# Performance work log

Measured on AMD Instinct MI355X. Metric: run time of the kernel, lower is better.

The kernel has to match this reference:

```python
import jax, jax.numpy as jnp
import numpy as np

EPS = 1e-6

def _layernorm2d(x, w, b):
    # normalize over channel dim (axis=1) per (b,h,w)
    u = jnp.mean(x, axis=1, keepdims=True)
    s = jnp.mean((x - u) ** 2, axis=1, keepdims=True)
    xn = (x - u) / jnp.sqrt(s + EPS)
    return xn * w[None, :, None, None] + b[None, :, None, None]

def _conv1x1(x, w, b):
    # w: (O, C, 1, 1)
    y = jnp.einsum('bchw,oc->bohw', x, w[:, :, 0, 0])
    return y + b[None, :, None, None]

def _dwconv3x3(x, w):
    # w: (C, 1, 3, 3), groups = C, padding 1, no bias
    C = x.shape[1]
    return jax.lax.conv_general_dilated(
        x, w, window_strides=(1, 1), padding=((1, 1), (1, 1)),
        dimension_numbers=('NCHW', 'OIHW', 'NCHW'), feature_group_count=C)

def _linrec_scan(a, u, axis):
    # s_t = a_t * s_{t-1} + u_t via associative scan
    def comb(l, r):
        al, ul = l
        ar, ur = r
        return al * ar, ar * ul + ur
    return jax.lax.associative_scan(comb, (a, u), axis=axis)[1]

def _bidir_scan(z, a, b, g, axis):
    u = b * z
    s_f = _linrec_scan(a, u, axis)
    s_b = jnp.flip(_linrec_scan(jnp.flip(a, axis), jnp.flip(u, axis), axis), axis)
    return g * (s_f + s_b)

def setup_inputs() -> dict:
    key = jax.random.key(0)
    ks = jax.random.split(key, 6)
    B, C, H, W = 8, 192, 128, 128
    x = jax.random.normal(ks[0], (B, C, H, W), dtype=jnp.float32)
    ln_w = jnp.ones((C,), jnp.float32)
    ln_b = jnp.zeros((C,), jnp.float32)
    dw_w = jax.random.normal(ks[1], (C, 1, 3, 3), jnp.float32) * (1.0 / 3.0)
    loc_w = jax.random.normal(ks[2], (C, C, 1, 1), jnp.float32) * (1.0 / np.sqrt(C))
    loc_b = jnp.zeros((C,), jnp.float32)
    par_w = jax.random.normal(ks[3], (3 * C, C, 1, 1), jnp.float32) * (1.0 / np.sqrt(C))
    par_b = jnp.zeros((3 * C,), jnp.float32)
    out_w = jax.random.normal(ks[4], (C, C, 1, 1), jnp.float32) * (1.0 / np.sqrt(C))
    out_b = jnp.zeros((C,), jnp.float32)
    return {"x": x, "ln_w": ln_w, "ln_b": ln_b, "dw_w": dw_w,
            "loc_w": loc_w, "loc_b": loc_b, "par_w": par_w, "par_b": par_b,
            "out_w": out_w, "out_b": out_b}

def reference(x, ln_w, ln_b, dw_w, loc_w, loc_b, par_w, par_b, out_w, out_b):
    C = x.shape[1]
    z = _layernorm2d(x, ln_w, ln_b)
    local_feat = _conv1x1(_dwconv3x3(z, dw_w), loc_w, loc_b)
    gates = _conv1x1(z, par_w, par_b)
    alpha = jax.nn.sigmoid(gates[:, :C])
    beta = jax.nn.sigmoid(gates[:, C:2 * C])
    gamma = jax.nn.sigmoid(gates[:, 2 * C:])
    y_w = _bidir_scan(z, alpha, beta, gamma, axis=3)  # along W
    y_h = _bidir_scan(z, alpha, beta, gamma, axis=2)  # along H
    y = local_feat + 0.5 * (y_w + y_h)
    y = jax.nn.silu(y)
    y = _conv1x1(y, out_w, out_b)
    return x + y
```

## Files before the change

kernel.cpp:

```cpp
#include <hip/hip_runtime.h>
#include <hip/hip_bf16.h>
#include <cstdint>
#include <cstddef>

#define B 8
#define C 192
#define H 128
#define W 128
#define HW (H * W)
#define CHW ((size_t)C * HW)
#define K C

typedef __attribute__((ext_vector_type(8))) short short8v;
typedef __attribute__((ext_vector_type(4))) float f32x4;
typedef __attribute__((ext_vector_type(4))) unsigned short ushort4v;

__device__ __forceinline__ float bf2f(unsigned short s) {
    union { float f; unsigned u; } cv; cv.u = ((unsigned)s) << 16; return cv.f;
}
__device__ __forceinline__ unsigned short f2bf(float f) {
    union { __hip_bfloat16 h; unsigned short u; } cv;
    cv.h = __float2bfloat16(f);
    return cv.u;
}

__global__ void prepack_kernel(const float* __restrict__ pw, const float* __restrict__ lw,
                               const float* __restrict__ ow, unsigned short* __restrict__ wb) {
    int i = blockIdx.x * 256 + threadIdx.x;
    const int NPW = 3 * C * K, NL = C * K;
    if (i < NPW) wb[i] = f2bf(pw[i]);
    else if (i < NPW + NL) wb[i] = f2bf(lw[i - NPW]);
    else if (i < NPW + 2 * NL) wb[i] = f2bf(ow[i - NPW - NL]);
}

__global__ __launch_bounds__(512, 4)
void lngates_kernel(const float* __restrict__ x, const float* __restrict__ lw,
                    const float* __restrict__ lb, const unsigned short* __restrict__ wb,
                    const float* __restrict__ bias, unsigned short* __restrict__ ZT,
                    unsigned short* __restrict__ PA, unsigned short* __restrict__ PU,
                    unsigned short* __restrict__ PG) {
    __shared__ char smem[96 * 384];
    __shared__ float stat[2][256];
    __shared__ float lwb[2][192];
    int tid = threadIdx.x;
    int p0 = blockIdx.x * 256;
    int bl = p0 >> 14, hwb = p0 & 16383;

    if (tid < 192) { lwb[0][tid] = lw[tid]; lwb[1][tid] = lb[tid]; }

    {
        float* part = (float*)smem;
        int px = tid & 255, half = tid >> 8;
        const float* xp = x + (size_t)bl * CHW + hwb + px;
        float sum = 0.f, sq = 0.f;
        for (int c = half * 96; c < half * 96 + 96; ++c) {
            float v = xp[(size_t)c * HW];
            sum += v; sq += v * v;
        }
        part[half * 256 + px] = sum;
        part[512 + half * 256 + px] = sq;
        __syncthreads();
        if (tid < 256) {
            float s = part[tid] + part[256 + tid];
            float q = part[512 + tid] + part[768 + tid];
            float mean = s * (1.0f / C);
            float var = fmaxf(q * (1.0f / C) - mean * mean, 0.f);
            stat[0][tid] = mean;
            stat[1][tid] = rsqrtf(var + 1e-6f);
        }
        __syncthreads();
    }

    int lane = tid & 63, wv = tid >> 6;
    int pw0 = p0 + wv * 32;
    int lr = lane & 15, lh = lane >> 4;
    int sw = (lr & 7) << 4;

    short8v bfr[2][6];
#pragma unroll
    for (int s = 0; s < 2; ++s) {
        int px = pw0 + s * 16 + lr;
        int hw = px & 16383;
        float mean = stat[0][px - p0], rs = stat[1][px - p0];
        const float* xp = x + (size_t)bl * CHW + hw;
#pragma unroll
        for (int t = 0; t < 6; ++t) {
            short8v v;
#pragma unroll
            for (int j = 0; j < 8; ++j) {
                int c = t * 32 + lh * 8 + j;
                float r = (xp[(size_t)c * HW] - mean) * rs * lwb[0][c] + lwb[1][c];
                v[j] = (short)f2bf(r);
            }
            bfr[s][t] = v;
            *(short8v*)(ZT + (size_t)px * K + t * 32 + lh * 8) = v;
        }
    }

    for (int gy = 0; gy < 3; ++gy) {
        for (int hf = 0; hf < 2; ++hf) {
            __syncthreads();
            const unsigned short* wsrc = wb + (size_t)gy * C * K + (size_t)hf * 96 * K;
#pragma unroll
            for (int it = 0; it < 5; ++it) {
                int e8 = it * 512 + tid;
                if (e8 < 2304) {
                    int row = e8 / 24;
                    int cb = (e8 % 24) * 16;
                    short8v v = *(const short8v*)(wsrc + e8 * 8);
                    *(short8v*)(smem + row * 384 + (cb ^ ((row & 7) << 4))) = v;
                }
            }
            __syncthreads();

            for (int otl = 0; otl < 6; ++otl) {
                int ot = hf * 6 + otl;
                int rb = (otl * 16 + lr) * 384;
                int o = ot * 16 + lr;
                f32x4 acc[2];
#pragma unroll
                for (int s = 0; s < 2; ++s) acc[s] = (f32x4){0.f, 0.f, 0.f, 0.f};
#pragma unroll
                for (int t = 0; t < 6; ++t) {
                    short8v af = *(const short8v*)(smem + rb + ((t * 64 + lh * 16) ^ sw));
#pragma unroll
                    for (int s = 0; s < 2; ++s)
                        acc[s] = __builtin_amdgcn_mfma_f32_16x16x32_bf16(bfr[s][t], af, acc[s], 0, 0, 0);
                }
                float bi = bias[gy * C + o];
#pragma unroll
                for (int s = 0; s < 2; ++s) {
                    int pst = pw0 + s * 16 + lh * 4;
                    int hw = pst & 16383;
                    ushort4v q;
#pragma unroll
                    for (int j = 0; j < 4; ++j) {
                        float v = acc[s][j] + bi;
                        v = 1.f / (1.f + __expf(-v));
                        if (gy == 1) v *= bf2f(ZT[(size_t)(pst + j) * K + o]);
                        q[j] = f2bf(v);
                    }
                    unsigned short* dst = (gy == 0) ? PA : ((gy == 1) ? PU : PG);
                    *(ushort4v*)(dst + (size_t)bl * CHW + (size_t)o * HW + hw) = q;
                }
            }
        }
    }
}

template <int MODE>
__global__ __launch_bounds__(256, 4)
void conv_mfma_kernel(const unsigned short* __restrict__ zt, const unsigned short* __restrict__ yin,
                      const unsigned short* __restrict__ wb, const float* __restrict__ bias,
                      const float* __restrict__ xres, float* __restrict__ Pf,
                      unsigned short* __restrict__ PA) {
    __shared__ char smem[96 * 384];
    int tid = threadIdx.x;
    int lane = tid & 63, wv = tid >> 6;
    int p0 = blockIdx.x * 128 + wv * 32;
    int lr = lane & 15, lh = lane >> 4;
    int sw = (lr & 7) << 4;

    short8v bfr[2][6];
    if (MODE != 2) {
#pragma unroll
        for (int s = 0; s < 2; ++s) {
            const unsigned short* zr = zt + (size_t)(p0 + s * 16 + lr) * K + lh * 8;
#pragma unroll
            for (int t = 0; t < 6; ++t) bfr[s][t] = *(const short8v*)(zr + t * 32);
        }
    } else {
        int bl = p0 >> 14, hwb = p0 & 16383;
        const unsigned short* yb = yin + (size_t)bl * CHW;
#pragma unroll
        for (int s = 0; s < 2; ++s) {
            int hw = hwb + s * 16 + lr;
#pragma unroll
            for (int t = 0; t < 6; ++t) {
                int c0 = t * 32 + lh * 8;
                short8v v;
#pragma unroll
                for (int j = 0; j < 8; ++j)
                    v[j] = (short)yb[(size_t)(c0 + j) * HW + hw];
                bfr[s][t] = v;
            }
        }
    }

    for (int hf = 0; hf < 2; ++hf) {
        __syncthreads();
        const unsigned short* wsrc = wb + (size_t)hf * 96 * K;
#pragma unroll
        for (int it = 0; it < 9; ++it) {
            int e8 = it * 256 + tid;
            int row = e8 / 24;
            int cb = (e8 % 24) * 16;
            short8v v = *(const short8v*)(wsrc + e8 * 8);
            *(short8v*)(smem + row * 384 + (cb ^ ((row & 7) << 4))) = v;
        }
        __syncthreads();

        for (int otl = 0; otl < 6; ++otl) {
            int ot = hf * 6 + otl;
            int rb = (otl * 16 + lr) * 384;
            int o = ot * 16 + lr;
            f32x4 acc[2];
#pragma unroll
            for (int s = 0; s < 2; ++s) acc[s] = (f32x4){0.f, 0.f, 0.f, 0.f};
#pragma unroll
            for (int t = 0; t < 6; ++t) {
                short8v af = *(const short8v*)(smem + rb + ((t * 64 + lh * 16) ^ sw));
#pragma unroll
                for (int s = 0; s < 2; ++s)
                    acc[s] = __builtin_amdgcn_mfma_f32_16x16x32_bf16(bfr[s][t], af, acc[s], 0, 0, 0);
            }
            float bi = bias[o];
#pragma unroll
            for (int s = 0; s < 2; ++s) {
                int pst = p0 + s * 16 + lh * 4;
                int bl = pst >> 14, hw = pst & 16383;
                if (MODE == 1) {
                    ushort4v q;
#pragma unroll
                    for (int j = 0; j < 4; ++j) q[j] = f2bf(acc[s][j] + bi);
                    *(ushort4v*)(PA + (size_t)bl * CHW + (size_t)o * HW + hw) = q;
                } else {
                    size_t ad = (size_t)bl * CHW + (size_t)o * HW + hw;
                    f32x4 x4 = *(const f32x4*)(xres + ad);
                    f32x4 q;
#pragma unroll
                    for (int j = 0; j < 4; ++j) q[j] = acc[s][j] + bi + x4[j];
                    *(f32x4*)(Pf + ad) = q;
                }
            }
        }
    }
}

#define TROWS 180
#define LPAD  392
__global__ __launch_bounds__(256, 2)
void dw3x3_kernel(const unsigned short* __restrict__ zt, const float* __restrict__ wgt,
                  unsigned short* __restrict__ dt) {
    __shared__ char lds[TROWS * LPAD];
    int tid = threadIdx.x;
    int bx = blockIdx.x;
    int bimg = bx >> 7;
    int rem = bx & 127;
    int th = rem >> 3, tw = rem & 7;
    int h0 = th * 8, w0 = tw * 16;
    size_t ibase = (size_t)bimg * HW;

    for (int e = tid; e < TROWS * 24; e += 256) {
        int row = e / 24, ch = e % 24;
        int hh = row / 18, ww = row % 18;
        int h = h0 - 1 + hh, w = w0 - 1 + ww;
        short8v v;
        if (h >= 0 && h < H && w >= 0 && w < W)
            v = *(const short8v*)(zt + (ibase + h * W + w) * K + ch * 8);
        else
            v = (short8v){0, 0, 0, 0, 0, 0, 0, 0};
        *(short8v*)(lds + row * LPAD + ch * 16) = v;
    }
    __syncthreads();

    int w_l = tid & 15, h_l = (tid >> 4) & 7, half = tid >> 7;
    int p_out = (h0 + h_l) * W + (w0 + w_l);
    unsigned short* dp = dt + (ibase + p_out) * K + half * 96;
#pragma unroll
    for (int cc = 0; cc < 12; ++cc) {
        int c8 = half * 12 + cc;
        float acc[8];
#pragma unroll
        for (int j = 0; j < 8; ++j) acc[j] = 0.f;
#pragma unroll
        for (int dy = -1; dy <= 1; ++dy) {
#pragma unroll
            for (int dx = -1; dx <= 1; ++dx) {
                int row = (h_l + 1 + dy) * 18 + (w_l + 1 + dx);
                short8v zv = *(const short8v*)(lds + row * LPAD + c8 * 16);
                int t = (dy + 1) * 3 + (dx + 1);
#pragma unroll
                for (int j = 0; j < 8; ++j)
                    acc[j] += wgt[(c8 * 8 + j) * 9 + t] * bf2f((unsigned short)zv[j]);
            }
        }
        short8v ov;
#pragma unroll
        for (int j = 0; j < 8; ++j) ov[j] = (short)f2bf(acc[j]);
        *(short8v*)(dp + cc * 8) = ov;
    }
}

__global__ __launch_bounds__(1024)
void scan_fused_kernel(const unsigned short* __restrict__ A_, const unsigned short* __restrict__ U_,
                       const unsigned short* __restrict__ G_, unsigned short* __restrict__ LY) {
    extern __shared__ float SMEM[];
    float* Sl = SMEM;
    unsigned* AU = (unsigned*)(SMEM + HW);
    float* CA = SMEM + 2 * HW;
    float* CU = CA + 1056;
    float* DA = CU + 1056;
    float* DU = DA + 1056;
    int tid = threadIdx.x;
    size_t pb = (size_t)blockIdx.x * HW;

    int h = tid >> 3, wc = tid & 7;
    int swzA = (h & 7) << 2;
    unsigned au[16];
    {
        const unsigned short* ap = A_ + pb + h * W + wc * 16;
        const unsigned short* up = U_ + pb + h * W + wc * 16;
        short8v a0 = *(const short8v*)ap, a1 = *(const short8v*)(ap + 8);
        short8v u0 = *(const short8v*)up, u1 = *(const short8v*)(up + 8);
#pragma unroll
        for (int i = 0; i < 8; ++i) {
            au[i]     = (unsigned)(unsigned short)a0[i] | ((unsigned)(unsigned short)u0[i] << 16);
            au[8 + i] = (unsigned)(unsigned short)a1[i] | ((unsigned)(unsigned short)u1[i] << 16);
        }
    }
#pragma unroll
    for (int i = 0; i < 16; ++i)
        AU[h * 128 + ((wc * 16 + i) ^ swzA)] = au[i];
    {
        float Af = 1.f, Uf = 0.f, Ab = 1.f, Ub = 0.f;
#pragma unroll
        for (int i = 0; i < 16; ++i) {
            float a = bf2f(au[i] & 0xffff), u = bf2f(au[i] >> 16);
            Uf = a * Uf + u; Af *= a;
        }
#pragma unroll
        for (int i = 15; i >= 0; --i) {
            float a = bf2f(au[i] & 0xffff), u = bf2f(au[i] >> 16);
            Ub = a * Ub + u; Ab *= a;
        }
        CA[wc * 132 + h] = Af; CU[wc * 132 + h] = Uf;
        DA[wc * 132 + h] = Ab; DU[wc * 132 + h] = Ub;
    }
    __syncthreads();

    if (tid < 128) {
        float s = 0.f;
#pragma unroll
        for (int k = 0; k < 8; ++k) {
            float Aa = CA[k * 132 + tid], Uu = CU[k * 132 + tid];
            CU[k * 132 + tid] = s;
            s = Aa * s + Uu;
        }
    } else if (tid < 256) {
        int hh = tid - 128;
        float s = 0.f;
#pragma unroll
        for (int k = 7; k >= 0; --k) {
            float Aa = DA[k * 132 + hh], Uu = DU[k * 132 + hh];
            DU[k * 132 + hh] = s;
            s = Aa * s + Uu;
        }
    }
    __syncthreads();

    {
        float sf = CU[wc * 132 + h];
        float sfa[16];
#pragma unroll
        for (int i = 0; i < 16; ++i) {
            float a = bf2f(au[i] & 0xffff), u = bf2f(au[i] >> 16);
            sf = a * sf + u; sfa[i] = sf;
        }
        float sb = DU[wc * 132 + h];
#pragma unroll
        for (int i = 15; i >= 0; --i) {
            float a = bf2f(au[i] & 0xffff), u = bf2f(au[i] >> 16);
            sb = a * sb + u;
            Sl[h * W + ((wc * 16 + i) ^ swzA)] = sfa[i] + sb;
        }
    }
    __syncthreads();

    int w = tid & 127, hc = tid >> 7;
    int h0 = hc * 16;
    unsigned au2[16];
#pragma unroll
    for (int i = 0; i < 16; ++i) {
        int hh = h0 + i;
        au2[i] = AU[hh * 128 + (w ^ ((hh & 7) << 2))];
    }
    {
        float Af = 1.f, Uf = 0.f, Ab = 1.f, Ub = 0.f;
#pragma unroll
        for (int i = 0; i < 16; ++i) {
            float a = bf2f(au2[i] & 0xffff), u = bf2f(au2[i] >> 16);
            Uf = a * Uf + u; Af *= a;
        }
#pragma unroll
        for (int i = 15; i >= 0; --i) {
            float a = bf2f(au2[i] & 0xffff), u = bf2f(au2[i] >> 16);
            Ub = a * Ub + u; Ab *= a;
        }
        CA[hc * 132 + w] = Af; CU[hc * 132 + w] = Uf;
        DA[hc * 132 + w] = Ab; DU[hc * 132 + w] = Ub;
    }
    __syncthreads();

    if (tid < 128) {
        float s = 0.f;
#pragma unroll
        for (int k = 0; k < 8; ++k) {
            float Aa = CA[k * 132 + tid], Uu = CU[k * 132 + tid];
            CU[k * 132 + tid] = s;
            s = Aa * s + Uu;
        }
    } else if (tid < 256) {
        int ww = tid - 128;
        float s = 0.f;
#pragma unroll
        for (int k = 7; k >= 0; --k) {
            float Aa = DA[k * 132 + ww], Uu = DU[k * 132 + ww];
            DU[k * 132 + ww] = s;
            s = Aa * s + Uu;
        }
    }
    __syncthreads();

    {
        float sf = CU[hc * 132 + w];
        float sfa[16];
#pragma unroll
        for (int i = 0; i < 16; ++i) {
            float a = bf2f(au2[i] & 0xffff), u = bf2f(au2[i] >> 16);
            sf = a * sf + u; sfa[i] = sf;
        }
        float sb = DU[hc * 132 + w];
#pragma unroll
        for (int i = 15; i >= 0; --i) {
            float a = bf2f(au2[i] & 0xffff), u = bf2f(au2[i] >> 16);
            sb = a * sb + u;
            int hh = h0 + i;
            size_t off = pb + (size_t)hh * W + w;
            float g = bf2f(G_[off]);
            float wsum = Sl[hh * W + (w ^ ((hh & 7) << 2))];
            float v = bf2f(LY[off]) + 0.5f * g * (wsum + sfa[i] + sb);
            LY[off] = f2bf(v / (1.f + __expf(-v)));
        }
    }
}

extern "C" void kernel_launch(void* const* d_in, const int* in_sizes, int n_in,
                              void* d_out, int out_size, void* d_ws, size_t ws_size,
                              hipStream_t stream) {
    const float* x     = (const float*)d_in[0];
    const float* ln_w  = (const float*)d_in[1];
    const float* ln_b  = (const float*)d_in[2];
    const float* dw_w  = (const float*)d_in[3];
    const float* loc_w = (const float*)d_in[4];
    const float* loc_b = (const float*)d_in[5];
    const float* par_w = (const float*)d_in[6];
    const float* par_b = (const float*)d_in[7];
    const float* out_w = (const float*)d_in[8];
    const float* out_b = (const float*)d_in[9];
    float* out = (float*)d_out;
    unsigned short* wsu = (unsigned short*)d_ws;

    const int WBN = 5 * C * K;
    int nb = 8;
    while (nb > 1) {
        size_t need = (size_t)WBN * 2 + (size_t)5 * nb * CHW * 2;
        if (need <= ws_size) break;
        nb >>= 1;
    }

    prepack_kernel<<<(WBN + 255) / 256, 256, 0, stream>>>(par_w, loc_w, out_w, wsu);

    const size_t SCAN_LDS = (size_t)(2 * HW + 4 * 1056) * 4;

    for (int b0 = 0; b0 < B; b0 += nb) {
        size_t ge = (size_t)nb * CHW;
        unsigned short* WB = wsu;
        unsigned short* Ab = wsu + WBN;
        unsigned short* Ub = Ab + ge;
        unsigned short* Gb = Ub + ge;
        unsigned short* ZT = Gb + ge;
        unsigned short* DT = ZT + ge;
        const float* xg = x + (size_t)b0 * CHW;
        int npg = nb * HW;

        lngates_kernel<<<npg / 256, 512, 0, stream>>>(
            xg, ln_w, ln_b, WB, par_b, ZT, Ab, Ub, Gb);
        dw3x3_kernel<<<nb * 128, 256, 0, stream>>>(ZT, dw_w, DT);
        conv_mfma_kernel<1><<<npg / 128, 256, 0, stream>>>(
            DT, nullptr, WB + 3 * C * K, loc_b, nullptr, nullptr, ZT);
        scan_fused_kernel<<<nb * C, 1024, SCAN_LDS, stream>>>(Ab, Ub, Gb, ZT);
        conv_mfma_kernel<2><<<npg / 128, 256, 0, stream>>>(
            nullptr, ZT, WB + 4 * C * K, out_b, xg, out + (size_t)b0 * CHW, nullptr);
    }
}
```

Baseline: 322.1 us.

## Fuse depthwise 3x3 conv with local 1x1 MFMA conv in one kernel

Merges the depthwise 3x3 kernel and the following 1x1 local projection into a single kernel. The depthwise output for an 8x8 pixel tile stays in swizzled LDS and feeds bf16 MFMA directly, with the weights streamed through LDS in two halves. This drops one full write and read of the intermediate tensor to global memory and one kernel launch. In exchange the tiles are smaller (8x8), which raises halo reload overhead, and each block now issues only modest MFMA work with more syncs, so reuse of the 1x1 weights per block goes down.

Result: slower. 340.4 us (+5.7%).

```diff
diff --git a/kernel.cpp b/kernel.cpp
--- a/kernel.cpp
+++ b/kernel.cpp
@@ -237,39 +237,39 @@
     }
 }
 
-#define TROWS 180
-#define LPAD  392
+#define DLPAD 392
+#define DWOUT_OFF 39200
 __global__ __launch_bounds__(256, 2)
-void dw3x3_kernel(const unsigned short* __restrict__ zt, const float* __restrict__ wgt,
-                  unsigned short* __restrict__ dt) {
-    __shared__ char lds[TROWS * LPAD];
+void dwloc_kernel(const unsigned short* __restrict__ zt, const float* __restrict__ wgt,
+                  const unsigned short* __restrict__ wb, const float* __restrict__ bias,
+                  unsigned short* __restrict__ LOC) {
+    __shared__ char lds[DWOUT_OFF + 64 * 384];
     int tid = threadIdx.x;
     int bx = blockIdx.x;
-    int bimg = bx >> 7;
-    int rem = bx & 127;
-    int th = rem >> 3, tw = rem & 7;
-    int h0 = th * 8, w0 = tw * 16;
+    int bimg = bx >> 8;
+    int rem = bx & 255;
+    int th = rem >> 4, tw = rem & 15;
+    int h0 = th * 8, w0 = tw * 8;
     size_t ibase = (size_t)bimg * HW;
 
-    for (int e = tid; e < TROWS * 24; e += 256) {
+    for (int e = tid; e < 100 * 24; e += 256) {
         int row = e / 24, ch = e % 24;
-        int hh = row / 18, ww = row % 18;
+        int hh = row / 10, ww = row % 10;
         int h = h0 - 1 + hh, w = w0 - 1 + ww;
         short8v v;
         if (h >= 0 && h < H && w >= 0 && w < W)
             v = *(const short8v*)(zt + (ibase + h * W + w) * K + ch * 8);
         else
             v = (short8v){0, 0, 0, 0, 0, 0, 0, 0};
-        *(short8v*)(lds + row * LPAD + ch * 16) = v;
-    }
-    __syncthreads();
-
-    int w_l = tid & 15, h_l = (tid >> 4) & 7, half = tid >> 7;
-    int p_out = (h0 + h_l) * W + (w0 + w_l);
-    unsigned short* dp = dt + (ibase + p_out) * K + half * 96;
-#pragma unroll
-    for (int cc = 0; cc < 12; ++cc) {
-        int c8 = half * 12 + cc;
+        *(short8v*)(lds + row * DLPAD + ch * 16) = v;
+    }
+    __syncthreads();
+
+    int lp = tid >> 2, qt = tid & 3;
+    int h_l = lp >> 3, w_l = lp & 7;
+#pragma unroll
+    for (int cc = 0; cc < 6; ++cc) {
+        int c8 = qt * 6 + cc;
         float acc[8];
 #pragma unroll
         for (int j = 0; j < 8; ++j) acc[j] = 0.f;
@@ -277,8 +277,8 @@
         for (int dy = -1; dy <= 1; ++dy) {
 #pragma unroll
             for (int dx = -1; dx <= 1; ++dx) {
-                int row = (h_l + 1 + dy) * 18 + (w_l + 1 + dx);
-                short8v zv = *(const short8v*)(lds + row * LPAD + c8 * 16);
+                int row = (h_l + 1 + dy) * 10 + (w_l + 1 + dx);
+                short8v zv = *(const short8v*)(lds + row * DLPAD + c8 * 16);
                 int t = (dy + 1) * 3 + (dx + 1);
 #pragma unroll
                 for (int j = 0; j < 8; ++j)
@@ -288,7 +288,51 @@
         short8v ov;
 #pragma unroll
         for (int j = 0; j < 8; ++j) ov[j] = (short)f2bf(acc[j]);
-        *(short8v*)(dp + cc * 8) = ov;
+        *(short8v*)(lds + DWOUT_OFF + lp * 384 + ((c8 * 16) ^ ((lp & 7) << 4))) = ov;
+    }
+    __syncthreads();
+
+    int lane = tid & 63, wv = tid >> 6;
+    int lr = lane & 15, lh = lane >> 4;
+    int sw = (lr & 7) << 4;
+    int prow = wv * 16 + lr;
+    short8v bfr[6];
+#pragma unroll
+    for (int t = 0; t < 6; ++t)
+        bfr[t] = *(const short8v*)(lds + DWOUT_OFF + prow * 384 +
+                                   ((t * 64 + lh * 16) ^ ((prow & 7) << 4)));
+
+    for (int hf = 0; hf < 2; ++hf) {
+        __syncthreads();
+        const unsigned short* wsrc = wb + (size_t)hf * 96 * K;
+#pragma unroll
+        for (int it = 0; it < 9; ++it) {
+            int e8 = it * 256 + tid;
+            int row = e8 / 24;
+            int cb = (e8 % 24) * 16;
+            short8v v = *(const short8v*)(wsrc + e8 * 8);
+            *(short8v*)(lds + row * 384 + (cb ^ ((row & 7) << 4))) = v;
+        }
+        __syncthreads();
+
+        for (int otl = 0; otl < 6; ++otl) {
+            int ot = hf * 6 + otl;
+            int rb = (otl * 16 + lr) * 384;
+            int o = ot * 16 + lr;
+            f32x4 acc = (f32x4){0.f, 0.f, 0.f, 0.f};
+#pragma unroll
+            for (int t = 0; t < 6; ++t) {
+                short8v af = *(const short8v*)(lds + rb + ((t * 64 + lh * 16) ^ sw));
+                acc = __builtin_amdgcn_mfma_f32_16x16x32_bf16(bfr[t], af, acc, 0, 0, 0);
+            }
+            float bi = bias[o];
+            int lq = wv * 16 + lh * 4;
+            int h = h0 + (lq >> 3), w = w0 + (lq & 7);
+            ushort4v q;
+#pragma unroll
+            for (int j = 0; j < 4; ++j) q[j] = f2bf(acc[j] + bi);
+            *(ushort4v*)(LOC + (size_t)bimg * CHW + (size_t)o * HW + h * W + w) = q;
+        }
     }
 }
 
@@ -486,11 +530,10 @@
 
         lngates_kernel<<<npg / 256, 512, 0, stream>>>(
             xg, ln_w, ln_b, WB, par_b, ZT, Ab, Ub, Gb);
-        dw3x3_kernel<<<nb * 128, 256, 0, stream>>>(ZT, dw_w, DT);
-        conv_mfma_kernel<1><<<npg / 128, 256, 0, stream>>>(
-            DT, nullptr, WB + 3 * C * K, loc_b, nullptr, nullptr, ZT);
-        scan_fused_kernel<<<nb * C, 1024, SCAN_LDS, stream>>>(Ab, Ub, Gb, ZT);
+        dwloc_kernel<<<nb * 256, 256, 0, stream>>>(
+            ZT, dw_w, WB + 3 * C * K, loc_b, DT);
+        scan_fused_kernel<<<nb * C, 1024, SCAN_LDS, stream>>>(Ab, Ub, Gb, DT);
         conv_mfma_kernel<2><<<npg / 128, 256, 0, stream>>>(
-            nullptr, ZT, WB + 4 * C * K, out_b, xg, out + (size_t)b0 * CHW, nullptr);
-    }
-}
+            nullptr, DT, WB + 4 * C * K, out_b, xg, out + (size_t)b0 * CHW, nullptr);
+    }
+}
```

## Double-buffer gate weight tiles in LDS for lngates GEMM

Applied to the files above, without the earlier changes.

Splits the gate weight staging into twelve 48-row chunks held in two LDS buffers, loading the next chunk while computing MFMAs on the current one, and issues the first chunk before the LN pass. This replaces the load-sync-compute-sync pattern per 96-row half with one barrier per stage. It is meant to hide global weight load latency behind compute, at the cost of more barriers overall and a loop with finer granularity.

Result: no change. 326.6 us (+1.4%).

```diff
diff --git a/kernel.cpp b/kernel.cpp
--- a/kernel.cpp
+++ b/kernel.cpp
@@ -39,7 +39,7 @@
                     const float* __restrict__ bias, unsigned short* __restrict__ ZT,
                     unsigned short* __restrict__ PA, unsigned short* __restrict__ PU,
                     unsigned short* __restrict__ PG) {
-    __shared__ char smem[96 * 384];
+    __shared__ char smem[2 * 48 * 384];
     __shared__ float stat[2][256];
     __shared__ float lwb[2][192];
     int tid = threadIdx.x;
@@ -71,6 +71,20 @@
         __syncthreads();
     }
 
+    {
+        const unsigned short* wsrc = wb;
+#pragma unroll
+        for (int it = 0; it < 3; ++it) {
+            int e8 = it * 512 + tid;
+            if (e8 < 1152) {
+                int row = e8 / 24;
+                int cb = (e8 % 24) * 16;
+                short8v v = *(const short8v*)(wsrc + e8 * 8);
+                *(short8v*)(smem + row * 384 + (cb ^ ((row & 7) << 4))) = v;
+            }
+        }
+    }
+
     int lane = tid & 63, wv = tid >> 6;
     int pw0 = p0 + wv * 32;
     int lr = lane & 15, lh = lane >> 4;
@@ -97,54 +111,57 @@
         }
     }
 
-    for (int gy = 0; gy < 3; ++gy) {
-        for (int hf = 0; hf < 2; ++hf) {
-            __syncthreads();
-            const unsigned short* wsrc = wb + (size_t)gy * C * K + (size_t)hf * 96 * K;
-#pragma unroll
-            for (int it = 0; it < 5; ++it) {
+    __syncthreads();
+
+    for (int st = 0; st < 12; ++st) {
+        char* cur = smem + (st & 1) * (48 * 384);
+        char* nxt = smem + ((st + 1) & 1) * (48 * 384);
+        if (st < 11) {
+            const unsigned short* wsrc = wb + (size_t)(st + 1) * 48 * K;
+#pragma unroll
+            for (int it = 0; it < 3; ++it) {
                 int e8 = it * 512 + tid;
-                if (e8 < 2304) {
+                if (e8 < 1152) {
                     int row = e8 / 24;
                     int cb = (e8 % 24) * 16;
                     short8v v = *(const short8v*)(wsrc + e8 * 8);
-                    *(short8v*)(smem + row * 384 + (cb ^ ((row & 7) << 4))) = v;
+                    *(short8v*)(nxt + row * 384 + (cb ^ ((row & 7) << 4))) = v;
                 }
             }
-            __syncthreads();
-
-            for (int otl = 0; otl < 6; ++otl) {
-                int ot = hf * 6 + otl;
-                int rb = (otl * 16 + lr) * 384;
-                int o = ot * 16 + lr;
-                f32x4 acc[2];
-#pragma unroll
-                for (int s = 0; s < 2; ++s) acc[s] = (f32x4){0.f, 0.f, 0.f, 0.f};
-#pragma unroll
-                for (int t = 0; t < 6; ++t) {
-                    short8v af = *(const short8v*)(smem + rb + ((t * 64 + lh * 16) ^ sw));
-#pragma unroll
-                    for (int s = 0; s < 2; ++s)
-                        acc[s] = __builtin_amdgcn_mfma_f32_16x16x32_bf16(bfr[s][t], af, acc[s], 0, 0, 0);
+        }
+        int gy = st >> 2;
+#pragma unroll
+        for (int otl = 0; otl < 3; ++otl) {
+            int rb = (otl * 16 + lr) * 384;
+            int o = (st & 3) * 48 + otl * 16 + lr;
+            f32x4 acc[2];
+#pragma unroll
+            for (int s = 0; s < 2; ++s) acc[s] = (f32x4){0.f, 0.f, 0.f, 0.f};
+#pragma unroll
+            for (int t = 0; t < 6; ++t) {
+                short8v af = *(const short8v*)(cur + rb + ((t * 64 + lh * 16) ^ sw));
+#pragma unroll
+                for (int s = 0; s < 2; ++s)
+                    acc[s] = __builtin_amdgcn_mfma_f32_16x16x32_bf16(bfr[s][t], af, acc[s], 0, 0, 0);
+            }
+            float bi = bias[gy * C + o];
+#pragma unroll
+            for (int s = 0; s < 2; ++s) {
+                int pst = pw0 + s * 16 + lh * 4;
+                int hw = pst & 16383;
+                ushort4v q;
+#pragma unroll
+                for (int j = 0; j < 4; ++j) {
+                    float v = acc[s][j] + bi;
+                    v = 1.f / (1.f + __expf(-v));
+                    if (gy == 1) v *= bf2f(ZT[(size_t)(pst + j) * K + o]);
+                    q[j] = f2bf(v);
                 }
-                float bi = bias[gy * C + o];
-#pragma unroll
-                for (int s = 0; s < 2; ++s) {
-                    int pst = pw0 + s * 16 + lh * 4;
-                    int hw = pst & 16383;
-                    ushort4v q;
-#pragma unroll
-                    for (int j = 0; j < 4; ++j) {
-                        float v = acc[s][j] + bi;
-                        v = 1.f / (1.f + __expf(-v));
-                        if (gy == 1) v *= bf2f(ZT[(size_t)(pst + j) * K + o]);
-                        q[j] = f2bf(v);
-                    }
-                    unsigned short* dst = (gy == 0) ? PA : ((gy == 1) ? PU : PG);
-                    *(ushort4v*)(dst + (size_t)bl * CHW + (size_t)o * HW + hw) = q;
-                }
-            }
-        }
+                unsigned short* dst = (gy == 0) ? PA : ((gy == 1) ? PU : PG);
+                *(ushort4v*)(dst + (size_t)bl * CHW + (size_t)o * HW + hw) = q;
+            }
+        }
+        __syncthreads();
     }
 }
 
```
